# Kernel tuning notes

Measured on AMD Instinct MI355X. Metric: run time of the kernel, lower is better.

## Reference

```python
import jax, jax.numpy as jnp
import numpy as np

ITERS = 10


def setup_inputs() -> dict:
    key = jax.random.key(0)
    k0, k1 = jax.random.split(key)
    B, D, H, W = 4, 64, 64, 64
    feat0 = jax.random.normal(k0, (B, D, H, W), dtype=jnp.float32)
    feat1 = jax.random.normal(k1, (B, D, H, W), dtype=jnp.float32)
    bin_score = jnp.asarray(1.0, dtype=jnp.float32)  # learned scalar parameter
    return {"feat0": feat0, "feat1": feat1, "bin_score": bin_score}


def _cdist(x, y):
    # torch.cdist(p=2): euclidean distance between rows. x: [b,m,d], y: [b,n,d]
    x2 = jnp.sum(x * x, axis=-1)[:, :, None]          # [b,m,1]
    y2 = jnp.sum(y * y, axis=-1)[:, None, :]          # [b,1,n]
    xy = jnp.einsum('bmd,bnd->bmn', x, y)             # [b,m,n]
    d2 = jnp.maximum(x2 + y2 - 2.0 * xy, 0.0)
    return jnp.sqrt(d2)


def _log_sinkhorn(Z, log_mu, log_nu, iters):
    # Z: [b, m+1, n+1]; log_mu: [b, m+1]; log_nu: [b, n+1]
    u0 = jnp.zeros_like(log_mu)
    v0 = jnp.zeros_like(log_nu)

    def body(i, uv):
        u, v = uv
        u = log_mu - jax.nn.logsumexp(Z + v[:, None, :], axis=2)
        v = log_nu - jax.nn.logsumexp(Z + u[:, :, None], axis=1)
        return (u, v)

    u, v = jax.lax.fori_loop(0, iters, body, (u0, v0))
    return Z + u[:, :, None] + v[:, None, :]


def _forward(feat0, feat1, bin_score):
    b, d, h, w = feat0.shape
    f0 = feat0.transpose(0, 2, 3, 1).reshape(b, h * w, d)
    f1 = feat1.transpose(0, 2, 3, 1).reshape(b, h * w, d)
    distance = _cdist(f0, f1)                         # [b, m, n]
    m, n = h * w, h * w
    dt = distance.dtype

    bins0 = jnp.broadcast_to(bin_score, (b, m, 1)).astype(dt)
    bins1 = jnp.broadcast_to(bin_score, (b, 1, n)).astype(dt)
    binsa = jnp.broadcast_to(bin_score, (b, 1, 1)).astype(dt)
    couplings = jnp.concatenate([
        jnp.concatenate([distance, bins0], axis=-1),
        jnp.concatenate([bins1, binsa], axis=-1),
    ], axis=1)                                        # [b, m+1, n+1]

    ms = jnp.asarray(m, dt)
    ns = jnp.asarray(n, dt)
    norm = -jnp.log(ms + ns)
    log_mu = jnp.concatenate([jnp.full((m,), norm, dtype=dt), (jnp.log(ns) + norm)[None]])
    log_nu = jnp.concatenate([jnp.full((n,), norm, dtype=dt), (jnp.log(ms) + norm)[None]])
    log_mu = jnp.broadcast_to(log_mu[None], (b, m + 1))
    log_nu = jnp.broadcast_to(log_nu[None], (b, n + 1))

    Z = _log_sinkhorn(couplings, log_mu, log_nu, ITERS)
    Z = Z - norm
    gamma = jnp.exp(Z)                                # [b, m+1, n+1]

    matching_loss = jnp.mean(jnp.sum(gamma[:, :-1, :-1] * distance, axis=2))
    dustbin_loss = jnp.mean(gamma[:, :, -1]) + jnp.mean(gamma[:, :-1, :])
    return matching_loss, dustbin_loss, gamma


def reference(feat0, feat1, bin_score):
    return _forward(feat0, feat1, bin_score)
```

## Files before the change

### kernel.cpp

```cpp
#include <hip/hip_runtime.h>
#include <math.h>

#define BB 4
#define DD 64
#define MM 4096
#define M1 4097
#define NORMC 9.0109133472792788f
#define CSH 11.0f
#define SCL8 1.0e12f
#define INVSCL8 1.0e-12f

typedef __attribute__((ext_vector_type(8))) short bf16x8;
typedef __attribute__((ext_vector_type(4))) float f32x4;

__device__ __forceinline__ f32x4 mfma16(bf16x8 a, bf16x8 b, f32x4 c) {
    return __builtin_amdgcn_mfma_f32_16x16x32_bf16(a, b, c, 0, 0, 0);
}
__device__ __forceinline__ unsigned short f2bf(float x) {
    unsigned u = __float_as_uint(x);
    u += 0x7fffu + ((u >> 16) & 1u);
    return (unsigned short)(u >> 16);
}
__device__ __forceinline__ float bf2f(unsigned short h) {
    return __uint_as_float(((unsigned)h) << 16);
}

__global__ void __launch_bounds__(256)
prep_kernel(const float* __restrict__ f0, const float* __restrict__ f1,
            unsigned short* __restrict__ h0, unsigned short* __restrict__ l0,
            unsigned short* __restrict__ h1, unsigned short* __restrict__ l1) {
    __shared__ float T[64][65];
    const int b = blockIdx.y;
    const int p0 = blockIdx.x * 64;
    const float* src = (blockIdx.z == 0 ? f0 : f1) + (size_t)b * DD * MM;
    unsigned short* dh = (blockIdx.z == 0 ? h0 : h1) + (size_t)b * MM * DD;
    unsigned short* dl = (blockIdx.z == 0 ? l0 : l1) + (size_t)b * MM * DD;
    const int tid = threadIdx.x;
#pragma unroll
    for (int l = 0; l < 16; ++l) {
        int idx = l * 256 + tid;
        T[idx >> 6][idx & 63] = src[(idx >> 6) * MM + p0 + (idx & 63)];
    }
    __syncthreads();
    const int p = tid >> 2;
    const int cs = (tid & 3) * 16;
    unsigned hw[8], lw[8];
#pragma unroll
    for (int k = 0; k < 8; ++k) {
        float x0 = T[cs + 2 * k][p], x1 = T[cs + 2 * k + 1][p];
        unsigned short a = f2bf(x0), c = f2bf(x1);
        hw[k] = (unsigned)a | ((unsigned)c << 16);
        unsigned short ra = f2bf(x0 - bf2f(a)), rc = f2bf(x1 - bf2f(c));
        lw[k] = (unsigned)ra | ((unsigned)rc << 16);
    }
    size_t base = (size_t)(p0 + p) * DD + cs;
    *(uint4*)(dh + base)     = make_uint4(hw[0], hw[1], hw[2], hw[3]);
    *(uint4*)(dh + base + 8) = make_uint4(hw[4], hw[5], hw[6], hw[7]);
    *(uint4*)(dl + base)     = make_uint4(lw[0], lw[1], lw[2], lw[3]);
    *(uint4*)(dl + base + 8) = make_uint4(lw[4], lw[5], lw[6], lw[7]);
}

__global__ void __launch_bounds__(256)
norms_kernel(const float* __restrict__ f0, const float* __restrict__ f1,
             float* __restrict__ n0, float* __restrict__ n1) {
    int t = blockIdx.x * 256 + threadIdx.x;
    if (t >= BB * MM) return;
    int b = t / MM, p = t % MM;
    const float* s0 = f0 + (size_t)b * DD * MM + p;
    const float* s1 = f1 + (size_t)b * DD * MM + p;
    float a = 0.f, c = 0.f;
#pragma unroll 8
    for (int k = 0; k < DD; ++k) {
        float x = s0[(size_t)k * MM]; a = fmaf(x, x, a);
        float y = s1[(size_t)k * MM]; c = fmaf(y, y, c);
    }
    n0[t] = a; n1[t] = c;
}

__global__ void __launch_bounds__(256)
init_kernel(float* __restrict__ W, float* __restrict__ S) {
    int t = blockIdx.x * 256 + threadIdx.x;
    if (t < BB * MM) W[t] = 1.0f;
    if (t < 8) S[t] = 1.0f;
}

__global__ void __launch_bounds__(256)
distEB_kernel(const unsigned short* __restrict__ h0, const unsigned short* __restrict__ l0,
              const unsigned short* __restrict__ h1, const unsigned short* __restrict__ l1,
              const float* __restrict__ n0, const float* __restrict__ n1,
              uint2* __restrict__ EB) {
    __shared__ unsigned char sc[4][640];
    const int id = blockIdx.x;
    const int xcd = id & 7, slot = id >> 3;
    const int b = xcd >> 1;
    const int x = slot * 2 + (xcd & 1);
    const int r0 = x * 32;
    const int tid = threadIdx.x;
    const int w = tid >> 6, l = tid & 63, lg = l >> 4, lc = l & 15;
    const size_t fb = (size_t)b * MM * DD;

    bf16x8 Ah[2][2], Al[2][2];
    float n0r[2][4];
#pragma unroll
    for (int st = 0; st < 2; ++st) {
        const unsigned short* pa = h0 + fb + (size_t)(r0 + st * 16 + lc) * DD + 8 * lg;
        const unsigned short* qa = l0 + fb + (size_t)(r0 + st * 16 + lc) * DD + 8 * lg;
        Ah[st][0] = *(const bf16x8*)pa; Ah[st][1] = *(const bf16x8*)(pa + 32);
        Al[st][0] = *(const bf16x8*)qa; Al[st][1] = *(const bf16x8*)(qa + 32);
#pragma unroll
        for (int e = 0; e < 4; ++e)
            n0r[st][e] = n0[b * MM + r0 + st * 16 + 4 * lg + e];
    }

    for (int tt = 0; tt < 64; ++tt) {
        const int jt = w * 64 + tt;
        const int j0 = jt * 16;
        const unsigned short* pb = h1 + fb + (size_t)(j0 + lc) * DD + 8 * lg;
        const unsigned short* qb = l1 + fb + (size_t)(j0 + lc) * DD + 8 * lg;
        bf16x8 Bh0 = *(const bf16x8*)pb, Bh1 = *(const bf16x8*)(pb + 32);
        bf16x8 Bl0 = *(const bf16x8*)qb, Bl1 = *(const bf16x8*)(qb + 32);
        float n1j = n1[b * MM + j0 + lc];
        unsigned pk[2];
#pragma unroll
        for (int st = 0; st < 2; ++st) {
            f32x4 acc = {0.f, 0.f, 0.f, 0.f};
            acc = mfma16(Ah[st][0], Bh0, acc);
            acc = mfma16(Ah[st][1], Bh1, acc);
            acc = mfma16(Ah[st][0], Bl0, acc);
            acc = mfma16(Ah[st][1], Bl1, acc);
            acc = mfma16(Al[st][0], Bh0, acc);
            acc = mfma16(Al[st][1], Bh1, acc);
            float Ev[4];
#pragma unroll
            for (int e = 0; e < 4; ++e) {
                float d2 = fmaxf(__builtin_fmaf(-2.f, acc[e], n0r[st][e] + n1j), 0.f);
                Ev[e] = __expf(sqrtf(d2) - CSH);
            }
            int p = __builtin_amdgcn_cvt_pk_fp8_f32(Ev[0], Ev[1], 0, false);
            p = __builtin_amdgcn_cvt_pk_fp8_f32(Ev[2], Ev[3], p, true);
            pk[st] = (unsigned)p;
        }
        *(unsigned*)&sc[w][lc * 40 + 4 * lg]      = pk[0];
        *(unsigned*)&sc[w][lc * 40 + 16 + 4 * lg] = pk[1];
        uint2 v = *(const uint2*)&sc[w][lc * 40 + 8 * lg];
        EB[(((size_t)(b * 128 + x)) * 256 + jt) * 64 + l] = v;
    }
}

__global__ void __launch_bounds__(512)
sinkEB_kernel(const uint2* __restrict__ EB, const float* __restrict__ W,
              float* __restrict__ X, float* __restrict__ S,
              float* __restrict__ psum, const float* __restrict__ bin) {
    const int bid = blockIdx.x;
    const int tid = threadIdx.x;
    const float bs = *bin;
    if (bid < BB) {
        __shared__ float am[8];
        const int b = bid;
        const int w = tid >> 6, l = tid & 63;
        float s = 0.f;
        for (int t = tid; t < MM; t += 512) s += W[b * MM + t];
#pragma unroll
        for (int off = 1; off < 64; off <<= 1) s += __shfl_xor(s, off);
        if (l == 0) am[w] = s;
        __syncthreads();
        if (tid == 0) {
            float tot = 0.f;
#pragma unroll
            for (int k = 0; k < 8; ++k) tot += am[k];
            S[b] = 0.5f * __expf(-bs) / (tot + S[4 + b]);
        }
        return;
    }
    __shared__ float Wl[4096];
    __shared__ float ps[256];
    __shared__ float XL[32];
    const int idx = bid - BB;
    const int b = idx >> 7, x = idx & 127;
    const int w = tid >> 6, l = tid & 63, lg = l >> 4, lc = l & 15;
    const float KC = __expf(-NORMC - CSH);
    const float wmm = __expf(bs - CSH) * S[4 + b];
#pragma unroll
    for (int k = 0; k < 8; ++k) Wl[k * 512 + tid] = W[b * MM + k * 512 + tid];
    __syncthreads();

    const uint2* EP = EB + (((size_t)(b * 128 + x)) * 256 + w * 32) * 64 + l;
    uint2 ec[32];
#pragma unroll
    for (int k = 0; k < 32; ++k) ec[k] = EP[(size_t)k * 64];

    float rs[8] = {};
#pragma unroll
    for (int k = 0; k < 32; ++k) {
        float wv = Wl[(w * 32 + k) * 16 + lc];
        auto p0 = __builtin_amdgcn_cvt_pk_f32_fp8((int)ec[k].x, false);
        auto p1 = __builtin_amdgcn_cvt_pk_f32_fp8((int)ec[k].x, true);
        auto p2 = __builtin_amdgcn_cvt_pk_f32_fp8((int)ec[k].y, false);
        auto p3 = __builtin_amdgcn_cvt_pk_f32_fp8((int)ec[k].y, true);
        rs[0] = fmaf(p0[0], wv, rs[0]); rs[1] = fmaf(p0[1], wv, rs[1]);
        rs[2] = fmaf(p1[0], wv, rs[2]); rs[3] = fmaf(p1[1], wv, rs[3]);
        rs[4] = fmaf(p2[0], wv, rs[4]); rs[5] = fmaf(p2[1], wv, rs[5]);
        rs[6] = fmaf(p3[0], wv, rs[6]); rs[7] = fmaf(p3[1], wv, rs[7]);
    }
#pragma unroll
    for (int off = 1; off < 16; off <<= 1)
#pragma unroll
        for (int t = 0; t < 8; ++t) rs[t] += __shfl_xor(rs[t], off);
    if (lc == 0) {
#pragma unroll
        for (int t = 0; t < 8; ++t) ps[w * 32 + 8 * lg + t] = rs[t];
    }
    __syncthreads();
    if (tid < 32) {
        float s = 0.f;
#pragma unroll
        for (int k = 0; k < 8; ++k) s += ps[k * 32 + tid];
        float xv = KC / (s + wmm);
        X[b * MM + x * 32 + tid] = xv;
        XL[tid] = xv * SCL8;
    }
    __syncthreads();

    float f0 = XL[8 * lg + 0], f1 = XL[8 * lg + 1];
    float f2 = XL[8 * lg + 2], f3 = XL[8 * lg + 3];
    float f4 = XL[8 * lg + 4], f5 = XL[8 * lg + 5];
    float f6 = XL[8 * lg + 6], f7 = XL[8 * lg + 7];
    int u0 = __builtin_amdgcn_cvt_pk_fp8_f32(f0, f1, 0, false);
    u0 = __builtin_amdgcn_cvt_pk_fp8_f32(f2, f3, u0, true);
    int u1 = __builtin_amdgcn_cvt_pk_fp8_f32(f4, f5, 0, false);
    u1 = __builtin_amdgcn_cvt_pk_fp8_f32(f6, f7, u1, true);
    long long av = (long long)(((unsigned long long)(unsigned)u1 << 32) | (unsigned)u0);
    float* po = psum + ((size_t)(b * 128 + x)) * MM;
    const f32x4 zero = {0.f, 0.f, 0.f, 0.f};
#pragma unroll
    for (int k = 0; k < 32; ++k) {
        long long bv = (long long)(((unsigned long long)ec[k].y << 32) | ec[k].x);
        f32x4 c = __builtin_amdgcn_mfma_f32_16x16x32_fp8_fp8(av, bv, zero, 0, 0, 0);
        if (l < 16) po[(w * 32 + k) * 16 + l] = c[0];
    }
}

__global__ void __launch_bounds__(256)
wcomb_kernel(const float* __restrict__ psum, const float* __restrict__ X,
             float* __restrict__ W, float* __restrict__ S,
             const float* __restrict__ bin) {
    const int bid = blockIdx.x;
    const int tid = threadIdx.x;
    const float bs = *bin;
    if (bid < BB * 64) {
        __shared__ float ps[256];
        const int b = bid >> 6, cg = bid & 63;
        const int c64 = tid & 63, g = tid >> 6;
        const float* pp = psum + ((size_t)(b * 128 + g * 32)) * MM + cg * 64 + c64;
        float s = 0.f;
#pragma unroll
        for (int c = 0; c < 32; ++c) s += pp[(size_t)c * MM];
        ps[tid] = s;
        __syncthreads();
        if (tid < 64) {
            float t = ps[tid] + ps[tid + 64] + ps[tid + 128] + ps[tid + 192];
            t = t * INVSCL8 + __expf(bs - CSH) * S[b];
            W[b * MM + cg * 64 + tid] = __expf(-NORMC - CSH) / t;
        }
    } else {
        const int b = bid - BB * 64;
        const int w = tid >> 6, l = tid & 63;
        __shared__ float am[4];
        float s = 0.f;
        for (int t = tid; t < MM; t += 256) s += X[b * MM + t];
#pragma unroll
        for (int off = 1; off < 64; off <<= 1) s += __shfl_xor(s, off);
        if (l == 0) am[w] = s;
        __syncthreads();
        if (tid == 0) {
            float tot = am[0] + am[1] + am[2] + am[3];
            S[4 + b] = 0.5f * __expf(-bs) / (tot + S[b]);
        }
    }
}

__global__ void __launch_bounds__(256)
finEB_kernel(const uint2* __restrict__ EB, const float* __restrict__ X,
             const float* __restrict__ W, float* __restrict__ G,
             float* __restrict__ pA) {
    __shared__ float T[256][36];
    __shared__ float Wl[4096];
    __shared__ float XL[32];
    const int bid = blockIdx.x;
    const int b = bid >> 7, x = bid & 127;
    const int tid = threadIdx.x;
    const int w = tid >> 6, l = tid & 63, lg = l >> 4, lc = l & 15;
#pragma unroll
    for (int k = 0; k < 16; ++k) Wl[k * 256 + tid] = W[b * MM + k * 256 + tid];
    if (tid < 32) XL[tid] = X[b * MM + x * 32 + tid] * __expf(NORMC + CSH);
    __syncthreads();

    const uint2* EBb = EB + ((size_t)(b * 128 + x)) * 256 * 64;
    float pm = 0.f, pr = 0.f;
    for (int ch = 0; ch < 16; ++ch) {
#pragma unroll
        for (int q = 0; q < 4; ++q) {
            const int jt = ch * 16 + w * 4 + q;
            uint2 ev = EBb[(size_t)jt * 64 + l];
            float wv = Wl[jt * 16 + lc];
            auto p0 = __builtin_amdgcn_cvt_pk_f32_fp8((int)ev.x, false);
            auto p1 = __builtin_amdgcn_cvt_pk_f32_fp8((int)ev.x, true);
            auto p2 = __builtin_amdgcn_cvt_pk_f32_fp8((int)ev.y, false);
            auto p3 = __builtin_amdgcn_cvt_pk_f32_fp8((int)ev.y, true);
            float Ef[8] = {p0[0], p0[1], p1[0], p1[1], p2[0], p2[1], p3[0], p3[1]};
            float g[8];
#pragma unroll
            for (int t = 0; t < 8; ++t) {
                g[t] = Ef[t] * XL[8 * lg + t] * wv;
                pm = fmaf(g[t], (Ef[t] > 0.f) ? (CSH + __logf(Ef[t])) : 0.f, pm);
                pr += g[t];
            }
            const int jl = (w * 4 + q) * 16 + lc;
            f32x4 v0 = {g[0], g[1], g[2], g[3]};
            f32x4 v1 = {g[4], g[5], g[6], g[7]};
            *(f32x4*)&T[jl][8 * lg]     = v0;
            *(f32x4*)&T[jl][8 * lg + 4] = v1;
        }
        __syncthreads();
        float* gb = G + ((size_t)(b * M1 + x * 32)) * M1 + ch * 256 + tid;
#pragma unroll
        for (int r = 0; r < 32; ++r) gb[(size_t)r * M1] = T[tid][r];
        __syncthreads();
    }
#pragma unroll
    for (int off = 1; off < 64; off <<= 1) {
        pm += __shfl_xor(pm, off);
        pr += __shfl_xor(pr, off);
    }
    __shared__ float s0[4], s1[4];
    if (l == 0) { s0[w] = pm; s1[w] = pr; }
    __syncthreads();
    if (tid == 0) {
        pA[bid * 2 + 0] = s0[0] + s0[1] + s0[2] + s0[3];
        pA[bid * 2 + 1] = s1[0] + s1[1] + s1[2] + s1[3];
    }
}

__global__ void __launch_bounds__(256)
fin_edge_kernel(const float* __restrict__ X, const float* __restrict__ W,
                const float* __restrict__ S, const float* __restrict__ bin,
                float* __restrict__ G, float* __restrict__ pB) {
    const float bs = *bin;
    const float CC = __expf(NORMC + bs);
    int t = blockIdx.x * 256 + threadIdx.x;
    float pc = 0.f, pr = 0.f;
    if (t < BB * M1) {
        int b = t / M1, j = t % M1;
        float wj = (j < MM) ? W[b * MM + j] : S[4 + b];
        float g = CC * S[b] * wj;
        G[((size_t)b * M1 + MM) * M1 + j] = g;
        if (j == MM) pc += g;
    } else if (t < BB * M1 + BB * MM) {
        int q = t - BB * M1;
        int b = q / MM, i = q % MM;
        float g = CC * X[b * MM + i] * S[4 + b];
        G[((size_t)b * M1 + i) * M1 + MM] = g;
        pc += g; pr += g;
    }
#pragma unroll
    for (int off = 1; off < 64; off <<= 1) {
        pc += __shfl_xor(pc, off);
        pr += __shfl_xor(pr, off);
    }
    __shared__ float s0[4], s1[4];
    int tid = threadIdx.x;
    if ((tid & 63) == 0) { s0[tid >> 6] = pc; s1[tid >> 6] = pr; }
    __syncthreads();
    if (tid == 0) {
        pB[blockIdx.x * 2 + 0] = s0[0] + s0[1] + s0[2] + s0[3];
        pB[blockIdx.x * 2 + 1] = s1[0] + s1[1] + s1[2] + s1[3];
    }
}

__global__ void __launch_bounds__(256)
reduce_out_kernel(const float* __restrict__ pA, int nA,
                  const float* __restrict__ pB, int nB, float* __restrict__ out) {
    const int tid = threadIdx.x;
    float pm = 0.f, prA = 0.f, pc = 0.f, prB = 0.f;
    for (int r = tid; r < nA; r += 256) { pm += pA[2 * r]; prA += pA[2 * r + 1]; }
    for (int r = tid; r < nB; r += 256) { pc += pB[2 * r]; prB += pB[2 * r + 1]; }
#pragma unroll
    for (int off = 1; off < 64; off <<= 1) {
        pm += __shfl_xor(pm, off);
        prA += __shfl_xor(prA, off);
        pc += __shfl_xor(pc, off);
        prB += __shfl_xor(prB, off);
    }
    __shared__ float a0[4], a1[4], a2[4], a3[4];
    if ((tid & 63) == 0) {
        int w = tid >> 6;
        a0[w] = pm; a1[w] = prA; a2[w] = pc; a3[w] = prB;
    }
    __syncthreads();
    if (tid == 0) {
        float PM = a0[0] + a0[1] + a0[2] + a0[3];
        float PRA = a1[0] + a1[1] + a1[2] + a1[3];
        float PC = a2[0] + a2[1] + a2[2] + a2[3];
        float PRB = a3[0] + a3[1] + a3[2] + a3[3];
        out[0] = PM / (4.0f * 4096.0f);
        out[1] = PC / (4.0f * 4097.0f) + (PRA + PRB) / (4.0f * 4096.0f * 4097.0f);
    }
}

extern "C" void kernel_launch(void* const* d_in, const int* in_sizes, int n_in,
                              void* d_out, int out_size, void* d_ws, size_t ws_size,
                              hipStream_t stream) {
    const float* feat0 = (const float*)d_in[0];
    const float* feat1 = (const float*)d_in[1];
    const float* bin   = (const float*)d_in[2];
    float* out = (float*)d_out;
    float* G   = out + 2;
    float* ws  = (float*)d_ws;

    const size_t OF_X   = 0;
    const size_t OF_W   = 16384;
    const size_t OF_S   = 32768;
    const size_t OF_PA  = 32832;
    const size_t OF_PB  = 34880;
    const size_t OF_N0  = 35152;
    const size_t OF_N1  = 51536;
    const size_t OF_PS  = 67920;
    const size_t OF_BF  = 2165072;
    const size_t OF_E8  = 4262224;

    float* X    = ws + OF_X;
    float* W    = ws + OF_W;
    float* S    = ws + OF_S;
    float* pA   = ws + OF_PA;
    float* pB   = ws + OF_PB;
    float* n0   = ws + OF_N0;
    float* n1   = ws + OF_N1;
    float* psum = ws + OF_PS;
    unsigned short* h0 = (unsigned short*)(ws + OF_BF);
    unsigned short* l0 = h0 + 1048576;
    unsigned short* h1 = l0 + 1048576;
    unsigned short* l1 = h1 + 1048576;
    uint2* EB = (uint2*)(ws + OF_E8);

    init_kernel<<<64, 256, 0, stream>>>(W, S);
    prep_kernel<<<dim3(64, BB, 2), 256, 0, stream>>>(feat0, feat1, h0, l0, h1, l1);
    norms_kernel<<<64, 256, 0, stream>>>(feat0, feat1, n0, n1);
    distEB_kernel<<<512, 256, 0, stream>>>(h0, l0, h1, l1, n0, n1, EB);
    for (int it = 0; it < 10; ++it) {
        sinkEB_kernel<<<BB + BB * 128, 512, 0, stream>>>(EB, W, X, S, psum, bin);
        wcomb_kernel<<<BB * 64 + BB, 256, 0, stream>>>(psum, X, W, S, bin);
    }
    finEB_kernel<<<512, 256, 0, stream>>>(EB, X, W, G, pA);
    fin_edge_kernel<<<129, 256, 0, stream>>>(X, W, S, bin, G, pB);
    reduce_out_kernel<<<1, 256, 0, stream>>>(pA, 512, pB, 129, out);
}
```

Before: 447.5 us.

## Use fp8 MFMA with transposed E copy for Sinkhorn row sums; fuse small kernels

The distance kernel now also writes a transposed fp8 copy of the exponentiated kernel (ET), laid out so the Sinkhorn row-sum step can run as fp8 MFMA against a quantised, scaled W vector. This replaces the scalar fp8-decode plus FMA loop. The init kernel is folded into the norms kernel, and the edge-fill kernel is folded into the final kernel as extra blocks, which removes two launches. In exchange, W is quantised to fp8, which costs precision, and the distance kernel writes a second E buffer and does byte-wise shared-memory transposes.

New measurement: 495.1 us. 10.6% more time.

```diff
diff --git a/kernel.cpp b/kernel.cpp
--- a/kernel.cpp
+++ b/kernel.cpp
@@ -7,8 +7,10 @@
 #define M1 4097
 #define NORMC 9.0109133472792788f
 #define CSH 11.0f
-#define SCL8 1.0e12f
-#define INVSCL8 1.0e-12f
+#define SCLX 1.0e12f
+#define INVSCLX 1.0e-12f
+#define SCLW 64.0f
+#define INVSCLW 0.015625f
 
 typedef __attribute__((ext_vector_type(8))) short bf16x8;
 typedef __attribute__((ext_vector_type(4))) float f32x4;
@@ -62,7 +64,8 @@
 
 __global__ void __launch_bounds__(256)
 norms_kernel(const float* __restrict__ f0, const float* __restrict__ f1,
-             float* __restrict__ n0, float* __restrict__ n1) {
+             float* __restrict__ n0, float* __restrict__ n1,
+             float* __restrict__ W, float* __restrict__ S) {
     int t = blockIdx.x * 256 + threadIdx.x;
     if (t >= BB * MM) return;
     int b = t / MM, p = t % MM;
@@ -75,12 +78,7 @@
         float y = s1[(size_t)k * MM]; c = fmaf(y, y, c);
     }
     n0[t] = a; n1[t] = c;
-}
-
-__global__ void __launch_bounds__(256)
-init_kernel(float* __restrict__ W, float* __restrict__ S) {
-    int t = blockIdx.x * 256 + threadIdx.x;
-    if (t < BB * MM) W[t] = 1.0f;
+    W[t] = 1.0f;
     if (t < 8) S[t] = 1.0f;
 }
 
@@ -88,8 +86,9 @@
 distEB_kernel(const unsigned short* __restrict__ h0, const unsigned short* __restrict__ l0,
               const unsigned short* __restrict__ h1, const unsigned short* __restrict__ l1,
               const float* __restrict__ n0, const float* __restrict__ n1,
-              uint2* __restrict__ EB) {
+              uint2* __restrict__ EB, uint2* __restrict__ ET) {
     __shared__ unsigned char sc[4][640];
+    __shared__ unsigned char sct[4][1280];
     const int id = blockIdx.x;
     const int xcd = id & 7, slot = id >> 3;
     const int b = xcd >> 1;
@@ -112,45 +111,60 @@
             n0r[st][e] = n0[b * MM + r0 + st * 16 + 4 * lg + e];
     }
 
-    for (int tt = 0; tt < 64; ++tt) {
-        const int jt = w * 64 + tt;
-        const int j0 = jt * 16;
-        const unsigned short* pb = h1 + fb + (size_t)(j0 + lc) * DD + 8 * lg;
-        const unsigned short* qb = l1 + fb + (size_t)(j0 + lc) * DD + 8 * lg;
-        bf16x8 Bh0 = *(const bf16x8*)pb, Bh1 = *(const bf16x8*)(pb + 32);
-        bf16x8 Bl0 = *(const bf16x8*)qb, Bl1 = *(const bf16x8*)(qb + 32);
-        float n1j = n1[b * MM + j0 + lc];
-        unsigned pk[2];
-#pragma unroll
-        for (int st = 0; st < 2; ++st) {
-            f32x4 acc = {0.f, 0.f, 0.f, 0.f};
-            acc = mfma16(Ah[st][0], Bh0, acc);
-            acc = mfma16(Ah[st][1], Bh1, acc);
-            acc = mfma16(Ah[st][0], Bl0, acc);
-            acc = mfma16(Ah[st][1], Bl1, acc);
-            acc = mfma16(Al[st][0], Bh0, acc);
-            acc = mfma16(Al[st][1], Bh1, acc);
-            float Ev[4];
-#pragma unroll
-            for (int e = 0; e < 4; ++e) {
-                float d2 = fmaxf(__builtin_fmaf(-2.f, acc[e], n0r[st][e] + n1j), 0.f);
-                Ev[e] = __expf(sqrtf(d2) - CSH);
+    for (int ttp = 0; ttp < 32; ++ttp) {
+#pragma unroll
+        for (int p = 0; p < 2; ++p) {
+            const int jt = w * 64 + ttp * 2 + p;
+            const int j0 = jt * 16;
+            const unsigned short* pb = h1 + fb + (size_t)(j0 + lc) * DD + 8 * lg;
+            const unsigned short* qb = l1 + fb + (size_t)(j0 + lc) * DD + 8 * lg;
+            bf16x8 Bh0 = *(const bf16x8*)pb, Bh1 = *(const bf16x8*)(pb + 32);
+            bf16x8 Bl0 = *(const bf16x8*)qb, Bl1 = *(const bf16x8*)(qb + 32);
+            float n1j = n1[b * MM + j0 + lc];
+            unsigned pk[2];
+#pragma unroll
+            for (int st = 0; st < 2; ++st) {
+                f32x4 acc = {0.f, 0.f, 0.f, 0.f};
+                acc = mfma16(Ah[st][0], Bh0, acc);
+                acc = mfma16(Ah[st][1], Bh1, acc);
+                acc = mfma16(Ah[st][0], Bl0, acc);
+                acc = mfma16(Ah[st][1], Bl1, acc);
+                acc = mfma16(Al[st][0], Bh0, acc);
+                acc = mfma16(Al[st][1], Bh1, acc);
+                float Ev[4];
+#pragma unroll
+                for (int e = 0; e < 4; ++e) {
+                    float d2 = fmaxf(__builtin_fmaf(-2.f, acc[e], n0r[st][e] + n1j), 0.f);
+                    Ev[e] = __expf(sqrtf(d2) - CSH);
+                }
+                int pkv = __builtin_amdgcn_cvt_pk_fp8_f32(Ev[0], Ev[1], 0, false);
+                pkv = __builtin_amdgcn_cvt_pk_fp8_f32(Ev[2], Ev[3], pkv, true);
+                pk[st] = (unsigned)pkv;
+                unsigned v = pk[st];
+                sct[w][(st * 16 + 4 * lg + 0) * 40 + p * 16 + lc] = (unsigned char)(v);
+                sct[w][(st * 16 + 4 * lg + 1) * 40 + p * 16 + lc] = (unsigned char)(v >> 8);
+                sct[w][(st * 16 + 4 * lg + 2) * 40 + p * 16 + lc] = (unsigned char)(v >> 16);
+                sct[w][(st * 16 + 4 * lg + 3) * 40 + p * 16 + lc] = (unsigned char)(v >> 24);
             }
-            int p = __builtin_amdgcn_cvt_pk_fp8_f32(Ev[0], Ev[1], 0, false);
-            p = __builtin_amdgcn_cvt_pk_fp8_f32(Ev[2], Ev[3], p, true);
-            pk[st] = (unsigned)p;
-        }
-        *(unsigned*)&sc[w][lc * 40 + 4 * lg]      = pk[0];
-        *(unsigned*)&sc[w][lc * 40 + 16 + 4 * lg] = pk[1];
-        uint2 v = *(const uint2*)&sc[w][lc * 40 + 8 * lg];
-        EB[(((size_t)(b * 128 + x)) * 256 + jt) * 64 + l] = v;
+            *(unsigned*)&sc[w][lc * 40 + 4 * lg]      = pk[0];
+            *(unsigned*)&sc[w][lc * 40 + 16 + 4 * lg] = pk[1];
+            uint2 v = *(const uint2*)&sc[w][lc * 40 + 8 * lg];
+            EB[(((size_t)(b * 128 + x)) * 256 + jt) * 64 + l] = v;
+        }
+        const int jj = w * 32 + ttp;
+#pragma unroll
+        for (int g = 0; g < 2; ++g) {
+            uint2 tv = *(const uint2*)&sct[w][(g * 16 + lc) * 40 + 8 * lg];
+            ET[(((size_t)(b * 256 + x * 2 + g)) * 128 + jj) * 64 + l] = tv;
+        }
     }
 }
 
 __global__ void __launch_bounds__(512)
-sinkEB_kernel(const uint2* __restrict__ EB, const float* __restrict__ W,
-              float* __restrict__ X, float* __restrict__ S,
-              float* __restrict__ psum, const float* __restrict__ bin) {
+sinkEB_kernel(const uint2* __restrict__ EB, const uint2* __restrict__ ET,
+              const float* __restrict__ W, float* __restrict__ X,
+              float* __restrict__ S, float* __restrict__ psum,
+              const float* __restrict__ bin) {
     const int bid = blockIdx.x;
     const int tid = threadIdx.x;
     const float bs = *bin;
@@ -172,7 +186,7 @@
         }
         return;
     }
-    __shared__ float Wl[4096];
+    __shared__ __align__(16) unsigned char WqL[4096];
     __shared__ float ps[256];
     __shared__ float XL[32];
     const int idx = bid - BB;
@@ -180,44 +194,46 @@
     const int w = tid >> 6, l = tid & 63, lg = l >> 4, lc = l & 15;
     const float KC = __expf(-NORMC - CSH);
     const float wmm = __expf(bs - CSH) * S[4 + b];
-#pragma unroll
-    for (int k = 0; k < 8; ++k) Wl[k * 512 + tid] = W[b * MM + k * 512 + tid];
-    __syncthreads();
-
-    const uint2* EP = EB + (((size_t)(b * 128 + x)) * 256 + w * 32) * 64 + l;
-    uint2 ec[32];
-#pragma unroll
-    for (int k = 0; k < 32; ++k) ec[k] = EP[(size_t)k * 64];
-
-    float rs[8] = {};
-#pragma unroll
-    for (int k = 0; k < 32; ++k) {
-        float wv = Wl[(w * 32 + k) * 16 + lc];
-        auto p0 = __builtin_amdgcn_cvt_pk_f32_fp8((int)ec[k].x, false);
-        auto p1 = __builtin_amdgcn_cvt_pk_f32_fp8((int)ec[k].x, true);
-        auto p2 = __builtin_amdgcn_cvt_pk_f32_fp8((int)ec[k].y, false);
-        auto p3 = __builtin_amdgcn_cvt_pk_f32_fp8((int)ec[k].y, true);
-        rs[0] = fmaf(p0[0], wv, rs[0]); rs[1] = fmaf(p0[1], wv, rs[1]);
-        rs[2] = fmaf(p1[0], wv, rs[2]); rs[3] = fmaf(p1[1], wv, rs[3]);
-        rs[4] = fmaf(p2[0], wv, rs[4]); rs[5] = fmaf(p2[1], wv, rs[5]);
-        rs[6] = fmaf(p3[0], wv, rs[6]); rs[7] = fmaf(p3[1], wv, rs[7]);
-    }
-#pragma unroll
-    for (int off = 1; off < 16; off <<= 1)
-#pragma unroll
-        for (int t = 0; t < 8; ++t) rs[t] += __shfl_xor(rs[t], off);
-    if (lc == 0) {
-#pragma unroll
-        for (int t = 0; t < 8; ++t) ps[w * 32 + 8 * lg + t] = rs[t];
+
+    {
+        const float* wb = W + b * MM + tid * 8;
+        float4 w0 = *(const float4*)wb;
+        float4 w1 = *(const float4*)(wb + 4);
+        int u0 = __builtin_amdgcn_cvt_pk_fp8_f32(w0.x * SCLW, w0.y * SCLW, 0, false);
+        u0 = __builtin_amdgcn_cvt_pk_fp8_f32(w0.z * SCLW, w0.w * SCLW, u0, true);
+        int u1 = __builtin_amdgcn_cvt_pk_fp8_f32(w1.x * SCLW, w1.y * SCLW, 0, false);
+        u1 = __builtin_amdgcn_cvt_pk_fp8_f32(w1.z * SCLW, w1.w * SCLW, u1, true);
+        *(uint2*)&WqL[tid * 8] = make_uint2((unsigned)u0, (unsigned)u1);
+    }
+    __syncthreads();
+
+    f32x4 accR0 = {0.f, 0.f, 0.f, 0.f};
+    f32x4 accR1 = {0.f, 0.f, 0.f, 0.f};
+    const uint2* ET0 = ET + (((size_t)(b * 256 + x * 2 + 0)) * 128 + w * 16) * 64 + l;
+    const uint2* ET1 = ET + (((size_t)(b * 256 + x * 2 + 1)) * 128 + w * 16) * 64 + l;
+#pragma unroll
+    for (int t16 = 0; t16 < 16; ++t16) {
+        uint2 wq = *(const uint2*)&WqL[w * 512 + t16 * 32 + 8 * lg];
+        long long av = (long long)(((unsigned long long)wq.y << 32) | wq.x);
+        uint2 e0 = ET0[(size_t)t16 * 64];
+        uint2 e1 = ET1[(size_t)t16 * 64];
+        long long b0 = (long long)(((unsigned long long)e0.y << 32) | e0.x);
+        long long b1 = (long long)(((unsigned long long)e1.y << 32) | e1.x);
+        accR0 = __builtin_amdgcn_mfma_f32_16x16x32_fp8_fp8(av, b0, accR0, 0, 0, 0);
+        accR1 = __builtin_amdgcn_mfma_f32_16x16x32_fp8_fp8(av, b1, accR1, 0, 0, 0);
+    }
+    if (l < 16) {
+        ps[w * 32 + l]      = accR0[0];
+        ps[w * 32 + 16 + l] = accR1[0];
     }
     __syncthreads();
     if (tid < 32) {
         float s = 0.f;
 #pragma unroll
         for (int k = 0; k < 8; ++k) s += ps[k * 32 + tid];
-        float xv = KC / (s + wmm);
+        float xv = KC / (s * INVSCLW + wmm);
         X[b * MM + x * 32 + tid] = xv;
-        XL[tid] = xv * SCL8;
+        XL[tid] = xv * SCLX;
     }
     __syncthreads();
 
@@ -231,10 +247,12 @@
     u1 = __builtin_amdgcn_cvt_pk_fp8_f32(f6, f7, u1, true);
     long long av = (long long)(((unsigned long long)(unsigned)u1 << 32) | (unsigned)u0);
     float* po = psum + ((size_t)(b * 128 + x)) * MM;
+    const uint2* EP = EB + (((size_t)(b * 128 + x)) * 256 + w * 32) * 64 + l;
     const f32x4 zero = {0.f, 0.f, 0.f, 0.f};
 #pragma unroll
     for (int k = 0; k < 32; ++k) {
-        long long bv = (long long)(((unsigned long long)ec[k].y << 32) | ec[k].x);
+        uint2 e = EP[(size_t)k * 64];
+        long long bv = (long long)(((unsigned long long)e.y << 32) | e.x);
         f32x4 c = __builtin_amdgcn_mfma_f32_16x16x32_fp8_fp8(av, bv, zero, 0, 0, 0);
         if (l < 16) po[(w * 32 + k) * 16 + l] = c[0];
     }
@@ -259,7 +277,7 @@
         __syncthreads();
         if (tid < 64) {
             float t = ps[tid] + ps[tid + 64] + ps[tid + 128] + ps[tid + 192];
-            t = t * INVSCL8 + __expf(bs - CSH) * S[b];
+            t = t * INVSCLX + __expf(bs - CSH) * S[b];
             W[b * MM + cg * 64 + tid] = __expf(-NORMC - CSH) / t;
         }
     } else {
@@ -281,14 +299,48 @@
 
 __global__ void __launch_bounds__(256)
 finEB_kernel(const uint2* __restrict__ EB, const float* __restrict__ X,
-             const float* __restrict__ W, float* __restrict__ G,
-             float* __restrict__ pA) {
+             const float* __restrict__ W, const float* __restrict__ S,
+             const float* __restrict__ bin, float* __restrict__ G,
+             float* __restrict__ pA, float* __restrict__ pB) {
+    const int bid = blockIdx.x;
+    const int tid = threadIdx.x;
+    if (bid >= BB * 128) {
+        const int eb = bid - BB * 128;
+        const float bs = *bin;
+        const float CC = __expf(NORMC + bs);
+        int t = eb * 256 + tid;
+        float pc = 0.f, pr = 0.f;
+        if (t < BB * M1) {
+            int b = t / M1, j = t % M1;
+            float wj = (j < MM) ? W[b * MM + j] : S[4 + b];
+            float g = CC * S[b] * wj;
+            G[((size_t)b * M1 + MM) * M1 + j] = g;
+            if (j == MM) pc += g;
+        } else if (t < BB * M1 + BB * MM) {
+            int q = t - BB * M1;
+            int b = q / MM, i = q % MM;
+            float g = CC * X[b * MM + i] * S[4 + b];
+            G[((size_t)b * M1 + i) * M1 + MM] = g;
+            pc += g; pr += g;
+        }
+#pragma unroll
+        for (int off = 1; off < 64; off <<= 1) {
+            pc += __shfl_xor(pc, off);
+            pr += __shfl_xor(pr, off);
+        }
+        __shared__ float e0[4], e1[4];
+        if ((tid & 63) == 0) { e0[tid >> 6] = pc; e1[tid >> 6] = pr; }
+        __syncthreads();
+        if (tid == 0) {
+            pB[eb * 2 + 0] = e0[0] + e0[1] + e0[2] + e0[3];
+            pB[eb * 2 + 1] = e1[0] + e1[1] + e1[2] + e1[3];
+        }
+        return;
+    }
     __shared__ float T[256][36];
     __shared__ float Wl[4096];
     __shared__ float XL[32];
-    const int bid = blockIdx.x;
     const int b = bid >> 7, x = bid & 127;
-    const int tid = threadIdx.x;
     const int w = tid >> 6, l = tid & 63, lg = l >> 4, lc = l & 15;
 #pragma unroll
     for (int k = 0; k < 16; ++k) Wl[k * 256 + tid] = W[b * MM + k * 256 + tid];
@@ -342,42 +394,6 @@
 }
 
 __global__ void __launch_bounds__(256)
-fin_edge_kernel(const float* __restrict__ X, const float* __restrict__ W,
-                const float* __restrict__ S, const float* __restrict__ bin,
-                float* __restrict__ G, float* __restrict__ pB) {
-    const float bs = *bin;
-    const float CC = __expf(NORMC + bs);
-    int t = blockIdx.x * 256 + threadIdx.x;
-    float pc = 0.f, pr = 0.f;
-    if (t < BB * M1) {
-        int b = t / M1, j = t % M1;
-        float wj = (j < MM) ? W[b * MM + j] : S[4 + b];
-        float g = CC * S[b] * wj;
-        G[((size_t)b * M1 + MM) * M1 + j] = g;
-        if (j == MM) pc += g;
-    } else if (t < BB * M1 + BB * MM) {
-        int q = t - BB * M1;
-        int b = q / MM, i = q % MM;
-        float g = CC * X[b * MM + i] * S[4 + b];
-        G[((size_t)b * M1 + i) * M1 + MM] = g;
-        pc += g; pr += g;
-    }
-#pragma unroll
-    for (int off = 1; off < 64; off <<= 1) {
-        pc += __shfl_xor(pc, off);
-        pr += __shfl_xor(pr, off);
-    }
-    __shared__ float s0[4], s1[4];
-    int tid = threadIdx.x;
-    if ((tid & 63) == 0) { s0[tid >> 6] = pc; s1[tid >> 6] = pr; }
-    __syncthreads();
-    if (tid == 0) {
-        pB[blockIdx.x * 2 + 0] = s0[0] + s0[1] + s0[2] + s0[3];
-        pB[blockIdx.x * 2 + 1] = s1[0] + s1[1] + s1[2] + s1[3];
-    }
-}
-
-__global__ void __launch_bounds__(256)
 reduce_out_kernel(const float* __restrict__ pA, int nA,
                   const float* __restrict__ pB, int nB, float* __restrict__ out) {
     const int tid = threadIdx.x;
@@ -427,6 +443,7 @@
     const size_t OF_PS  = 67920;
     const size_t OF_BF  = 2165072;
     const size_t OF_E8  = 4262224;
+    const size_t OF_ET  = 21039440;
 
     float* X    = ws + OF_X;
     float* W    = ws + OF_W;
@@ -441,16 +458,15 @@
     unsigned short* h1 = l0 + 1048576;
     unsigned short* l1 = h1 + 1048576;
     uint2* EB = (uint2*)(ws + OF_E8);
-
-    init_kernel<<<64, 256, 0, stream>>>(W, S);
+    uint2* ET = (uint2*)(ws + OF_ET);
+
     prep_kernel<<<dim3(64, BB, 2), 256, 0, stream>>>(feat0, feat1, h0, l0, h1, l1);
-    norms_kernel<<<64, 256, 0, stream>>>(feat0, feat1, n0, n1);
-    distEB_kernel<<<512, 256, 0, stream>>>(h0, l0, h1, l1, n0, n1, EB);
+    norms_kernel<<<64, 256, 0, stream>>>(feat0, feat1, n0, n1, W, S);
+    distEB_kernel<<<512, 256, 0, stream>>>(h0, l0, h1, l1, n0, n1, EB, ET);
     for (int it = 0; it < 10; ++it) {
-        sinkEB_kernel<<<BB + BB * 128, 512, 0, stream>>>(EB, W, X, S, psum, bin);
+        sinkEB_kernel<<<BB + BB * 128, 512, 0, stream>>>(EB, ET, W, X, S, psum, bin);
         wcomb_kernel<<<BB * 64 + BB, 256, 0, stream>>>(psum, X, W, S, bin);
     }
-    finEB_kernel<<<512, 256, 0, stream>>>(EB, X, W, G, pA);
-    fin_edge_kernel<<<129, 256, 0, stream>>>(X, W, S, bin, G, pB);
-    reduce_out_kernel<<<1, 256, 0, stream>>>(pA, 512, pB, 129, out);
-}
+    finEB_kernel<<<BB * 128 + 129, 256, 0, stream>>>(EB, X, W, S, bin, G, pA, pB);
+    reduce_out_kernel<<<1, 256, 0, stream>>>(pA, BB * 128, pB, 129, out);
+}
```

## Drop bf16 split-precision correction terms and fuse init and edge kernels

Applied to the files above, without the earlier changes.

Removes the low-order bf16 residual arrays and their four extra MFMA ops per tile, so the distance GEMM uses only single bf16 operands. Folds the W/S initialisation into the norms kernel and merges the dustbin-edge kernel into the final EB kernel as extra blocks, removing two launches. The precision drop lowers distance accuracy, which is then exponentiated. That risks tolerance failures, since the activations are now computed with less precision than the reference requires.

Result: faster. 384.0 us (-14.2%).

```diff
diff --git a/kernel.cpp b/kernel.cpp
--- a/kernel.cpp
+++ b/kernel.cpp
@@ -7,8 +7,8 @@
 #define M1 4097
 #define NORMC 9.0109133472792788f
 #define CSH 11.0f
-#define SCL8 1.0e12f
-#define INVSCL8 1.0e-12f
+#define SCLX 1.0e12f
+#define INVSCLX 1.0e-12f
 
 typedef __attribute__((ext_vector_type(8))) short bf16x8;
 typedef __attribute__((ext_vector_type(4))) float f32x4;
@@ -21,20 +21,15 @@
     u += 0x7fffu + ((u >> 16) & 1u);
     return (unsigned short)(u >> 16);
 }
-__device__ __forceinline__ float bf2f(unsigned short h) {
-    return __uint_as_float(((unsigned)h) << 16);
-}
 
 __global__ void __launch_bounds__(256)
 prep_kernel(const float* __restrict__ f0, const float* __restrict__ f1,
-            unsigned short* __restrict__ h0, unsigned short* __restrict__ l0,
-            unsigned short* __restrict__ h1, unsigned short* __restrict__ l1) {
+            unsigned short* __restrict__ h0, unsigned short* __restrict__ h1) {
     __shared__ float T[64][65];
     const int b = blockIdx.y;
     const int p0 = blockIdx.x * 64;
     const float* src = (blockIdx.z == 0 ? f0 : f1) + (size_t)b * DD * MM;
     unsigned short* dh = (blockIdx.z == 0 ? h0 : h1) + (size_t)b * MM * DD;
-    unsigned short* dl = (blockIdx.z == 0 ? l0 : l1) + (size_t)b * MM * DD;
     const int tid = threadIdx.x;
 #pragma unroll
     for (int l = 0; l < 16; ++l) {
@@ -44,25 +39,22 @@
     __syncthreads();
     const int p = tid >> 2;
     const int cs = (tid & 3) * 16;
-    unsigned hw[8], lw[8];
+    unsigned hw[8];
 #pragma unroll
     for (int k = 0; k < 8; ++k) {
-        float x0 = T[cs + 2 * k][p], x1 = T[cs + 2 * k + 1][p];
-        unsigned short a = f2bf(x0), c = f2bf(x1);
+        unsigned short a = f2bf(T[cs + 2 * k][p]);
+        unsigned short c = f2bf(T[cs + 2 * k + 1][p]);
         hw[k] = (unsigned)a | ((unsigned)c << 16);
-        unsigned short ra = f2bf(x0 - bf2f(a)), rc = f2bf(x1 - bf2f(c));
-        lw[k] = (unsigned)ra | ((unsigned)rc << 16);
     }
     size_t base = (size_t)(p0 + p) * DD + cs;
     *(uint4*)(dh + base)     = make_uint4(hw[0], hw[1], hw[2], hw[3]);
     *(uint4*)(dh + base + 8) = make_uint4(hw[4], hw[5], hw[6], hw[7]);
-    *(uint4*)(dl + base)     = make_uint4(lw[0], lw[1], lw[2], lw[3]);
-    *(uint4*)(dl + base + 8) = make_uint4(lw[4], lw[5], lw[6], lw[7]);
 }
 
 __global__ void __launch_bounds__(256)
 norms_kernel(const float* __restrict__ f0, const float* __restrict__ f1,
-             float* __restrict__ n0, float* __restrict__ n1) {
+             float* __restrict__ n0, float* __restrict__ n1,
+             float* __restrict__ W, float* __restrict__ S) {
     int t = blockIdx.x * 256 + threadIdx.x;
     if (t >= BB * MM) return;
     int b = t / MM, p = t % MM;
@@ -75,18 +67,12 @@
         float y = s1[(size_t)k * MM]; c = fmaf(y, y, c);
     }
     n0[t] = a; n1[t] = c;
-}
-
-__global__ void __launch_bounds__(256)
-init_kernel(float* __restrict__ W, float* __restrict__ S) {
-    int t = blockIdx.x * 256 + threadIdx.x;
-    if (t < BB * MM) W[t] = 1.0f;
+    W[t] = 1.0f;
     if (t < 8) S[t] = 1.0f;
 }
 
 __global__ void __launch_bounds__(256)
-distEB_kernel(const unsigned short* __restrict__ h0, const unsigned short* __restrict__ l0,
-              const unsigned short* __restrict__ h1, const unsigned short* __restrict__ l1,
+distEB_kernel(const unsigned short* __restrict__ h0, const unsigned short* __restrict__ h1,
               const float* __restrict__ n0, const float* __restrict__ n1,
               uint2* __restrict__ EB) {
     __shared__ unsigned char sc[4][640];
@@ -99,14 +85,12 @@
     const int w = tid >> 6, l = tid & 63, lg = l >> 4, lc = l & 15;
     const size_t fb = (size_t)b * MM * DD;
 
-    bf16x8 Ah[2][2], Al[2][2];
+    bf16x8 Ah[2][2];
     float n0r[2][4];
 #pragma unroll
     for (int st = 0; st < 2; ++st) {
         const unsigned short* pa = h0 + fb + (size_t)(r0 + st * 16 + lc) * DD + 8 * lg;
-        const unsigned short* qa = l0 + fb + (size_t)(r0 + st * 16 + lc) * DD + 8 * lg;
         Ah[st][0] = *(const bf16x8*)pa; Ah[st][1] = *(const bf16x8*)(pa + 32);
-        Al[st][0] = *(const bf16x8*)qa; Al[st][1] = *(const bf16x8*)(qa + 32);
 #pragma unroll
         for (int e = 0; e < 4; ++e)
             n0r[st][e] = n0[b * MM + r0 + st * 16 + 4 * lg + e];
@@ -116,9 +100,7 @@
         const int jt = w * 64 + tt;
         const int j0 = jt * 16;
         const unsigned short* pb = h1 + fb + (size_t)(j0 + lc) * DD + 8 * lg;
-        const unsigned short* qb = l1 + fb + (size_t)(j0 + lc) * DD + 8 * lg;
         bf16x8 Bh0 = *(const bf16x8*)pb, Bh1 = *(const bf16x8*)(pb + 32);
-        bf16x8 Bl0 = *(const bf16x8*)qb, Bl1 = *(const bf16x8*)(qb + 32);
         float n1j = n1[b * MM + j0 + lc];
         unsigned pk[2];
 #pragma unroll
@@ -126,10 +108,6 @@
             f32x4 acc = {0.f, 0.f, 0.f, 0.f};
             acc = mfma16(Ah[st][0], Bh0, acc);
             acc = mfma16(Ah[st][1], Bh1, acc);
-            acc = mfma16(Ah[st][0], Bl0, acc);
-            acc = mfma16(Ah[st][1], Bl1, acc);
-            acc = mfma16(Al[st][0], Bh0, acc);
-            acc = mfma16(Al[st][1], Bh1, acc);
             float Ev[4];
 #pragma unroll
             for (int e = 0; e < 4; ++e) {
@@ -217,7 +195,7 @@
         for (int k = 0; k < 8; ++k) s += ps[k * 32 + tid];
         float xv = KC / (s + wmm);
         X[b * MM + x * 32 + tid] = xv;
-        XL[tid] = xv * SCL8;
+        XL[tid] = xv * SCLX;
     }
     __syncthreads();
 
@@ -259,7 +237,7 @@
         __syncthreads();
         if (tid < 64) {
             float t = ps[tid] + ps[tid + 64] + ps[tid + 128] + ps[tid + 192];
-            t = t * INVSCL8 + __expf(bs - CSH) * S[b];
+            t = t * INVSCLX + __expf(bs - CSH) * S[b];
             W[b * MM + cg * 64 + tid] = __expf(-NORMC - CSH) / t;
         }
     } else {
@@ -281,14 +259,48 @@
 
 __global__ void __launch_bounds__(256)
 finEB_kernel(const uint2* __restrict__ EB, const float* __restrict__ X,
-             const float* __restrict__ W, float* __restrict__ G,
-             float* __restrict__ pA) {
+             const float* __restrict__ W, const float* __restrict__ S,
+             const float* __restrict__ bin, float* __restrict__ G,
+             float* __restrict__ pA, float* __restrict__ pB) {
+    const int bid = blockIdx.x;
+    const int tid = threadIdx.x;
+    if (bid >= BB * 128) {
+        const int eb = bid - BB * 128;
+        const float bs = *bin;
+        const float CC = __expf(NORMC + bs);
+        int t = eb * 256 + tid;
+        float pc = 0.f, pr = 0.f;
+        if (t < BB * M1) {
+            int b = t / M1, j = t % M1;
+            float wj = (j < MM) ? W[b * MM + j] : S[4 + b];
+            float g = CC * S[b] * wj;
+            G[((size_t)b * M1 + MM) * M1 + j] = g;
+            if (j == MM) pc += g;
+        } else if (t < BB * M1 + BB * MM) {
+            int q = t - BB * M1;
+            int b = q / MM, i = q % MM;
+            float g = CC * X[b * MM + i] * S[4 + b];
+            G[((size_t)b * M1 + i) * M1 + MM] = g;
+            pc += g; pr += g;
+        }
+#pragma unroll
+        for (int off = 1; off < 64; off <<= 1) {
+            pc += __shfl_xor(pc, off);
+            pr += __shfl_xor(pr, off);
+        }
+        __shared__ float e0[4], e1[4];
+        if ((tid & 63) == 0) { e0[tid >> 6] = pc; e1[tid >> 6] = pr; }
+        __syncthreads();
+        if (tid == 0) {
+            pB[eb * 2 + 0] = e0[0] + e0[1] + e0[2] + e0[3];
+            pB[eb * 2 + 1] = e1[0] + e1[1] + e1[2] + e1[3];
+        }
+        return;
+    }
     __shared__ float T[256][36];
     __shared__ float Wl[4096];
     __shared__ float XL[32];
-    const int bid = blockIdx.x;
     const int b = bid >> 7, x = bid & 127;
-    const int tid = threadIdx.x;
     const int w = tid >> 6, l = tid & 63, lg = l >> 4, lc = l & 15;
 #pragma unroll
     for (int k = 0; k < 16; ++k) Wl[k * 256 + tid] = W[b * MM + k * 256 + tid];
@@ -342,42 +354,6 @@
 }
 
 __global__ void __launch_bounds__(256)
-fin_edge_kernel(const float* __restrict__ X, const float* __restrict__ W,
-                const float* __restrict__ S, const float* __restrict__ bin,
-                float* __restrict__ G, float* __restrict__ pB) {
-    const float bs = *bin;
-    const float CC = __expf(NORMC + bs);
-    int t = blockIdx.x * 256 + threadIdx.x;
-    float pc = 0.f, pr = 0.f;
-    if (t < BB * M1) {
-        int b = t / M1, j = t % M1;
-        float wj = (j < MM) ? W[b * MM + j] : S[4 + b];
-        float g = CC * S[b] * wj;
-        G[((size_t)b * M1 + MM) * M1 + j] = g;
-        if (j == MM) pc += g;
-    } else if (t < BB * M1 + BB * MM) {
-        int q = t - BB * M1;
-        int b = q / MM, i = q % MM;
-        float g = CC * X[b * MM + i] * S[4 + b];
-        G[((size_t)b * M1 + i) * M1 + MM] = g;
-        pc += g; pr += g;
-    }
-#pragma unroll
-    for (int off = 1; off < 64; off <<= 1) {
-        pc += __shfl_xor(pc, off);
-        pr += __shfl_xor(pr, off);
-    }
-    __shared__ float s0[4], s1[4];
-    int tid = threadIdx.x;
-    if ((tid & 63) == 0) { s0[tid >> 6] = pc; s1[tid >> 6] = pr; }
-    __syncthreads();
-    if (tid == 0) {
-        pB[blockIdx.x * 2 + 0] = s0[0] + s0[1] + s0[2] + s0[3];
-        pB[blockIdx.x * 2 + 1] = s1[0] + s1[1] + s1[2] + s1[3];
-    }
-}
-
-__global__ void __launch_bounds__(256)
 reduce_out_kernel(const float* __restrict__ pA, int nA,
                   const float* __restrict__ pB, int nB, float* __restrict__ out) {
     const int tid = threadIdx.x;
@@ -421,12 +397,12 @@
     const size_t OF_W   = 16384;
     const size_t OF_S   = 32768;
     const size_t OF_PA  = 32832;
-    const size_t OF_PB  = 34880;
-    const size_t OF_N0  = 35152;
-    const size_t OF_N1  = 51536;
-    const size_t OF_PS  = 67920;
-    const size_t OF_BF  = 2165072;
-    const size_t OF_E8  = 4262224;
+    const size_t OF_PB  = 33856;
+    const size_t OF_N0  = 34128;
+    const size_t OF_N1  = 50512;
+    const size_t OF_PS  = 66896;
+    const size_t OF_BF  = 2164048;
+    const size_t OF_E8  = 3212624;
 
     float* X    = ws + OF_X;
     float* W    = ws + OF_W;
@@ -437,20 +413,16 @@
     float* n1   = ws + OF_N1;
     float* psum = ws + OF_PS;
     unsigned short* h0 = (unsigned short*)(ws + OF_BF);
-    unsigned short* l0 = h0 + 1048576;
-    unsigned short* h1 = l0 + 1048576;
-    unsigned short* l1 = h1 + 1048576;
+    unsigned short* h1 = h0 + 1048576;
     uint2* EB = (uint2*)(ws + OF_E8);
 
-    init_kernel<<<64, 256, 0, stream>>>(W, S);
-    prep_kernel<<<dim3(64, BB, 2), 256, 0, stream>>>(feat0, feat1, h0, l0, h1, l1);
-    norms_kernel<<<64, 256, 0, stream>>>(feat0, feat1, n0, n1);
-    distEB_kernel<<<512, 256, 0, stream>>>(h0, l0, h1, l1, n0, n1, EB);
+    prep_kernel<<<dim3(64, BB, 2), 256, 0, stream>>>(feat0, feat1, h0, h1);
+    norms_kernel<<<64, 256, 0, stream>>>(feat0, feat1, n0, n1, W, S);
+    distEB_kernel<<<512, 256, 0, stream>>>(h0, h1, n0, n1, EB);
     for (int it = 0; it < 10; ++it) {
         sinkEB_kernel<<<BB + BB * 128, 512, 0, stream>>>(EB, W, X, S, psum, bin);
         wcomb_kernel<<<BB * 64 + BB, 256, 0, stream>>>(psum, X, W, S, bin);
     }
-    finEB_kernel<<<512, 256, 0, stream>>>(EB, X, W, G, pA);
-    fin_edge_kernel<<<129, 256, 0, stream>>>(X, W, S, bin, G, pB);
-    reduce_out_kernel<<<1, 256, 0, stream>>>(pA, 512, pB, 129, out);
-}
+    finEB_kernel<<<BB * 128 + 129, 256, 0, stream>>>(EB, X, W, S, bin, G, pA, pB);
+    reduce_out_kernel<<<1, 256, 0, stream>>>(pA, BB * 128, pB, 129, out);
+}
```
